# Kernel tuning notes

Measured on AMD Instinct MI355X. Metric: run time of the kernel, lower is better.

## Reference

```python
import jax, jax.numpy as jnp
import numpy as np

N_NODES = 100000
N_EDGES = 1600000
N_GRAPHS = 1024
F = 128
L = 3  # num_gnn_layers
EPS = 1e-5


def _ln(x, g, b):
    mu = jnp.mean(x, axis=-1, keepdims=True)
    v = jnp.mean((x - mu) ** 2, axis=-1, keepdims=True)
    return (x - mu) * jax.lax.rsqrt(v + EPS) * g + b


def setup_inputs() -> dict:
    key = jax.random.key(0)
    ks = jax.random.split(key, 40)
    s = 0.05
    d = {}
    d['x'] = jax.random.normal(ks[0], (N_NODES, F), jnp.float32)
    d['w'] = jax.random.uniform(ks[1], (N_NODES, 1), jnp.float32)
    d['edge_index'] = jax.random.randint(ks[2], (2, N_EDGES), 0, N_NODES)
    d['batch'] = jnp.sort(jax.random.randint(ks[3], (N_NODES,), 0, N_GRAPHS))
    # input linear: (monomer_features+1) -> gc_features
    d['W_in'] = jax.random.normal(ks[4], (F + 1, F), jnp.float32) * s
    d['b_in'] = jnp.zeros((F,), jnp.float32)
    # stacked GCBlock params [L, ...]
    d['sage_Wl'] = jax.random.normal(ks[5], (L, F, F), jnp.float32) * s
    d['sage_bl'] = jnp.zeros((L, F), jnp.float32)
    d['sage_Wr'] = jax.random.normal(ks[6], (L, F, F), jnp.float32) * s
    d['ln1_g'] = jnp.ones((L, F), jnp.float32)
    d['ln1_b'] = jnp.zeros((L, F), jnp.float32)
    d['lin1_W'] = jax.random.normal(ks[7], (L, F, F), jnp.float32) * s
    d['lin1_b'] = jnp.zeros((L, F), jnp.float32)
    d['lin2_W'] = jax.random.normal(ks[8], (L, F, F), jnp.float32) * s
    d['lin2_b'] = jnp.zeros((L, F), jnp.float32)
    d['ln2_g'] = jnp.ones((L, F), jnp.float32)
    d['ln2_b'] = jnp.zeros((L, F), jnp.float32)
    # MeanDiffFeatureBlock: Linear(2F -> F)
    d['mdf_W'] = jax.random.normal(ks[9], (2 * F, F), jnp.float32) * s
    d['mdf_b'] = jnp.zeros((F,), jnp.float32)
    # mean PoolingLayer params
    d['pln1_g'] = jnp.ones((F,), jnp.float32)
    d['pln1_b'] = jnp.zeros((F,), jnp.float32)
    d['plin1_W'] = jax.random.normal(ks[10], (F, F), jnp.float32) * s
    d['plin1_b'] = jnp.zeros((F,), jnp.float32)
    d['plin2_W'] = jax.random.normal(ks[11], (F, F), jnp.float32) * s
    d['plin2_b'] = jnp.zeros((F,), jnp.float32)
    d['pln2_g'] = jnp.ones((F,), jnp.float32)
    d['pln2_b'] = jnp.zeros((F,), jnp.float32)
    return d


def reference(x, w, edge_index, batch, W_in, b_in, sage_Wl, sage_bl, sage_Wr,
              ln1_g, ln1_b, lin1_W, lin1_b, lin2_W, lin2_b, ln2_g, ln2_b,
              mdf_W, mdf_b, pln1_g, pln1_b, plin1_W, plin1_b, plin2_W, plin2_b,
              pln2_g, pln2_b):
    src, dst = edge_index[0], edge_index[1]
    # in-degree for SAGE mean aggregation (clamped so isolated nodes -> 0 agg)
    deg = jax.ops.segment_sum(jnp.ones((N_EDGES,), jnp.float32), dst,
                              num_segments=N_NODES)
    deg = jnp.maximum(deg, 1.0)[:, None]
    # graph sizes for global_mean_pool
    cnt = jax.ops.segment_sum(jnp.ones((N_NODES,), jnp.float32), batch,
                              num_segments=N_GRAPHS)
    cnt = jnp.maximum(cnt, 1.0)[:, None]

    # inilinear on [x, weight-fraction]  (scalers are identity at init)
    h = jnp.concatenate([x, w], axis=-1) @ W_in + b_in  # [N, F]

    def gc_block(h, p):
        Wl, bl, Wr, g1, b1, W1, bb1, W2, bb2, g2, b2 = p
        # SAGEConv: lin_l(mean_j x_j) + lin_r(x_i)
        agg = jax.ops.segment_sum(h[src], dst, num_segments=N_NODES) / deg
        y = agg @ Wl + bl + h @ Wr
        y1 = _ln(y + h, g1, b1)
        y2 = jax.nn.elu(y1 @ W1 + bb1) @ W2 + bb2  # dropout = identity (eval)
        return _ln(y2 + y1, g2, b2), None

    h, _ = jax.lax.scan(gc_block, h,
                        (sage_Wl, sage_bl, sage_Wr, ln1_g, ln1_b,
                         lin1_W, lin1_b, lin2_W, lin2_b, ln2_g, ln2_b))

    # MeanDiffFeatureBlock
    gm = jax.ops.segment_sum(h, batch, num_segments=N_GRAPHS) / cnt  # [B, F]
    h = jnp.concatenate([h, h - gm[batch]], axis=-1) @ mdf_W + mdf_b

    # mean PoolingLayer
    p = jax.ops.segment_sum(h, batch, num_segments=N_GRAPHS) / cnt  # [B, F]
    hh = _ln(p, pln1_g, pln1_b)
    y = jax.nn.elu(hh @ plin1_W + plin1_b) @ plin2_W + plin2_b
    return _ln(y + hh, pln2_g, pln2_b)  # [B, F]
```

## Files before the change

### kernel.cpp

```cpp
#include <hip/hip_runtime.h>
#include <math.h>

#define NN 100000
#define NE 1600000
#define NG 1024
#define FF 128
#define BSH 9
#define NBK ((NN + 511) >> BSH)
#define RB 256
#define BCAP 16384

typedef __attribute__((ext_vector_type(8))) short short8;
typedef __attribute__((ext_vector_type(4))) float f32x4;
typedef __attribute__((ext_vector_type(2))) float f32x2;

__device__ __forceinline__ unsigned short f2b(float f) {
    union { float f; unsigned u; } v; v.f = f;
    unsigned r = (v.u + 0x7FFF + ((v.u >> 16) & 1)) >> 16;
    return (unsigned short)r;
}
__device__ __forceinline__ float us2f(unsigned short u) {
    union { unsigned u; float f; } v; v.u = ((unsigned)u) << 16; return v.f;
}
__device__ __forceinline__ float fast_elu(float v) {
    float e = __builtin_amdgcn_exp2f(v * 1.44269504088896340736f) - 1.0f;
    return v > 0.f ? v : e;
}
__device__ __forceinline__ uint2 pk8(const float* v) {
    unsigned lo = 0, hi = 0;
    lo = (unsigned)__builtin_amdgcn_cvt_pk_fp8_f32(v[0], v[1], (int)lo, false);
    lo = (unsigned)__builtin_amdgcn_cvt_pk_fp8_f32(v[2], v[3], (int)lo, true);
    hi = (unsigned)__builtin_amdgcn_cvt_pk_fp8_f32(v[4], v[5], (int)hi, false);
    hi = (unsigned)__builtin_amdgcn_cvt_pk_fp8_f32(v[6], v[7], (int)hi, true);
    uint2 r; r.x = lo; r.y = hi; return r;
}
#define MFMA(a, b, c) __builtin_amdgcn_mfma_f32_16x16x32_bf16((a), (b), (c), 0, 0, 0)

__global__ __launch_bounds__(256)
void radix_scatter(const int* __restrict__ src, const int* __restrict__ dst,
                   int* __restrict__ bcur, unsigned* __restrict__ pairs, int n) {
    __shared__ int base[NBK];
    __shared__ int cnt[NBK];
    for (int i = threadIdx.x; i < NBK; i += 256) cnt[i] = 0;
    __syncthreads();
    const int per = (n + RB - 1) / RB;
    const int beg = blockIdx.x * per;
    const int end = min(n, beg + per);
    for (int i = beg + threadIdx.x; i < end; i += 256)
        atomicAdd(&cnt[dst[i] >> BSH], 1);
    __syncthreads();
    for (int i = threadIdx.x; i < NBK; i += 256)
        base[i] = cnt[i] ? atomicAdd(&bcur[i], cnt[i]) : 0;
    __syncthreads();
    for (int i = beg + threadIdx.x; i < end; i += 256) {
        int d = dst[i];
        int p = atomicAdd(&base[d >> BSH], 1);
        pairs[p] = ((unsigned)src[i] << BSH) | (unsigned)(d & 511);
    }
}

__global__ __launch_bounds__(256)
void bucket_build(const unsigned* __restrict__ pairs, const int* __restrict__ bcur,
                  int* __restrict__ row_beg, int* __restrict__ row_end,
                  float* __restrict__ inv_deg, int* __restrict__ ssrc) {
    __shared__ int cnt[512];
    __shared__ int curs[512];
    __shared__ int wsum[4];
    const int b = blockIdx.x;
    const int n0 = b << BSH;
    const int t = threadIdx.x;
    const int lane = t & 63, wid = t >> 6;

    for (int i = t; i < 512; i += 256) cnt[i] = 0;
    __syncthreads();
    const int beg = b * BCAP, end = bcur[b];
    for (int i = beg + t; i < end; i += 256)
        atomicAdd(&cnt[pairs[i] & 511], 1);
    __syncthreads();

    int c0 = cnt[2 * t], c1 = cnt[2 * t + 1];
    int v = c0 + c1;
    int x = v;
    #pragma unroll
    for (int o = 1; o < 64; o <<= 1) {
        int y = __shfl_up(x, o);
        if (lane >= o) x += y;
    }
    if (lane == 63) wsum[wid] = x;
    __syncthreads();
    if (t == 0) {
        int s = 0;
        #pragma unroll
        for (int w2 = 0; w2 < 4; ++w2) { int tv = wsum[w2]; wsum[w2] = s; s += tv; }
    }
    __syncthreads();
    int g0 = beg + wsum[wid] + x - v;
    int g1 = g0 + c0;
    curs[2 * t] = g0;
    curs[2 * t + 1] = g1;
    {
        int node = n0 + 2 * t;
        if (node < NN) {
            row_beg[node] = g0; row_end[node] = g1;
            inv_deg[node] = 1.0f / (float)(c0 > 1 ? c0 : 1);
        }
        node = n0 + 2 * t + 1;
        if (node < NN) {
            row_beg[node] = g1; row_end[node] = g1 + c1;
            inv_deg[node] = 1.0f / (float)(c1 > 1 ? c1 : 1);
        }
    }
    __syncthreads();
    for (int i = beg + t; i < end; i += 256) {
        unsigned pr = pairs[i];
        int p = atomicAdd(&curs[pr & 511], 1);
        ssrc[p] = (int)(pr >> BSH) << 7;
    }
}

__global__ __launch_bounds__(256)
void graph_offsets(const int* __restrict__ batch, int* __restrict__ g_off,
                   float* __restrict__ inv_cnt, int* __restrict__ bcur) {
    int g = blockIdx.x * blockDim.x + threadIdx.x;
    if (g < NBK) bcur[g] = g * BCAP;
    if (g > NG) return;
    if (g == NG) { g_off[NG] = NN; return; }
    int lo = 0, hi = NN;
    while (lo < hi) { int mid = (lo + hi) >> 1; if (batch[mid] < g) lo = mid + 1; else hi = mid; }
    int lo2 = lo, hi2 = NN;
    while (lo2 < hi2) { int mid = (lo2 + hi2) >> 1; if (batch[mid] < g + 1) lo2 = mid + 1; else hi2 = mid; }
    g_off[g] = lo;
    int c = lo2 - lo;
    inv_cnt[g] = 1.0f / (float)(c > 1 ? c : 1);
}

struct WTab { const float* a[16]; };
__global__ __launch_bounds__(256)
void prep_weights(WTab tab, unsigned short* __restrict__ dst) {
    int w = blockIdx.x >> 6;
    int idx = ((blockIdx.x & 63) << 8) + threadIdx.x;
    int j = idx & 7, lane = (idx >> 3) & 63, nt = (idx >> 9) & 7, kc = idx >> 12;
    int cb = lane & 15, rq = lane >> 4;
    int k = kc * 32 + rq * 8 + j;
    int n = nt * 16 + cb;
    dst[(size_t)w * 16384 + idx] = f2b(tab.a[w][k * 128 + n]);
}

__global__ __launch_bounds__(256)
void sage_agg(const unsigned char* __restrict__ h8, const int* __restrict__ row_beg,
              const int* __restrict__ row_end, const float* __restrict__ inv_deg,
              const int* __restrict__ ssrc, unsigned short* __restrict__ aggb) {
    const int wid = threadIdx.x >> 6;
    const int lane = threadIdx.x & 63;
    const int node = blockIdx.x * 4 + wid;
    const int eg = lane >> 4, j = lane & 15;
    const int jo = j * 8;
    const int beg = row_beg[node], end = row_end[node];
    f32x2 a0 = {0.f, 0.f}, a1 = {0.f, 0.f}, a2 = {0.f, 0.f}, a3 = {0.f, 0.f};
    for (int e = beg + eg; e < end; e += 32) {
        uint2 u[8];
        #pragma unroll
        for (int k = 0; k < 8; ++k) {
            int ek = e + 4 * k;
            bool ok = ek < end;
            int idx = ssrc[ok ? ek : e];
            uint2 uu = *(const uint2*)(h8 + (unsigned)(idx + jo));
            uu.x = ok ? uu.x : 0u;
            uu.y = ok ? uu.y : 0u;
            u[k] = uu;
        }
        #pragma unroll
        for (int k = 0; k < 8; ++k) {
            a0 += __builtin_amdgcn_cvt_pk_f32_fp8(u[k].x, false);
            a1 += __builtin_amdgcn_cvt_pk_f32_fp8(u[k].x, true);
            a2 += __builtin_amdgcn_cvt_pk_f32_fp8(u[k].y, false);
            a3 += __builtin_amdgcn_cvt_pk_f32_fp8(u[k].y, true);
        }
    }
    float af[8] = {a0.x, a0.y, a1.x, a1.y, a2.x, a2.y, a3.x, a3.y};
    #pragma unroll
    for (int k = 0; k < 8; ++k) {
        af[k] += __shfl_xor(af[k], 16);
        af[k] += __shfl_xor(af[k], 32);
    }
    if (eg == 0) {
        float id = inv_deg[node];
        #pragma unroll
        for (int nt = 0; nt < 8; ++nt)
            aggb[(size_t)node * 128 + nt * 16 + j] = f2b(af[nt] * id);
    }
}

__global__ __launch_bounds__(64)
void pool_mean_b(const unsigned short* __restrict__ src, const int* __restrict__ g_off,
                 const float* __restrict__ inv_cnt, float* __restrict__ out) {
    const int g = blockIdx.x;
    const int lane = threadIdx.x & 63;
    const int j = lane & 15, rs = lane >> 4;
    const int beg = g_off[g], end = g_off[g + 1];
    float s[8] = {0.f, 0.f, 0.f, 0.f, 0.f, 0.f, 0.f, 0.f};
    for (int n = beg + rs; n < end; n += 4) {
        short8 v = *(const short8*)&src[(size_t)n * FF + j * 8];
        #pragma unroll
        for (int i = 0; i < 8; ++i) s[i] += us2f((unsigned short)v[i]);
    }
    #pragma unroll
    for (int i = 0; i < 8; ++i) {
        s[i] += __shfl_xor(s[i], 16);
        s[i] += __shfl_xor(s[i], 32);
    }
    if (rs == 0) {
        float ic = inv_cnt[g];
        #pragma unroll
        for (int i = 0; i < 8; ++i) out[(size_t)g * FF + j * 8 + i] = s[i] * ic;
    }
}

template<bool AB16, bool R1, int RESM, int ACT, bool LN, bool OF32, bool OB16, bool OB8>
__global__ __launch_bounds__(256)
void gemm_mfma(const void* __restrict__ A_,
               const unsigned short* __restrict__ Wf,
               const float* __restrict__ bias,
               const float* __restrict__ rvec, const float* __restrict__ rrow,
               const float* __restrict__ res,
               const float* __restrict__ lng, const float* __restrict__ lnb,
               float* __restrict__ outf, unsigned short* __restrict__ outb,
               unsigned char* __restrict__ outb8, int M) {
    __shared__ short Al[64 * 136];

    const int t = threadIdx.x;
    const int lane = t & 63, wid = t >> 6;
    const int m0 = blockIdx.x * 64;
    const int cb = lane & 15, rq = lane >> 4;

    if (AB16) {
        const unsigned short* Ab = (const unsigned short*)A_;
        for (int i = t; i < 1024; i += 256) {
            int row = i >> 4, seg = i & 15;
            int gr = m0 + row; if (gr >= M) gr = M - 1;
            *(uint4*)&Al[row * 136 + seg * 8] = *(const uint4*)&Ab[(size_t)gr * 128 + seg * 8];
        }
    } else {
        const float* Af = (const float*)A_;
        for (int i = t; i < 2048; i += 256) {
            int row = i >> 5, seg = i & 31;
            int gr = m0 + row; if (gr >= M) gr = M - 1;
            float4 v = *(const float4*)&Af[(size_t)gr * 128 + seg * 4];
            ushort4 o = {f2b(v.x), f2b(v.y), f2b(v.z), f2b(v.w)};
            *(ushort4*)&Al[row * 136 + seg * 4] = o;
        }
    }
    __syncthreads();

    f32x4 acc[8];
    #pragma unroll
    for (int nt = 0; nt < 8; ++nt) acc[nt] = (f32x4){0.f, 0.f, 0.f, 0.f};

    const int aoff_base = (wid * 16 + cb) * 136 + rq * 8;
    for (int kc = 0; kc < 4; ++kc) {
        short8 a0 = *(const short8*)&Al[aoff_base + kc * 32];
        #pragma unroll
        for (int nt = 0; nt < 8; ++nt) {
            short8 b0 = *(const short8*)&Wf[(size_t)(kc * 8 + nt) * 512 + lane * 8];
            acc[nt] = MFMA(a0, b0, acc[nt]);
        }
    }

    float bs[8], rr[8], lg[8], lb[8];
    #pragma unroll
    for (int nt = 0; nt < 8; ++nt) {
        int col = nt * 16 + cb;
        bs[nt] = bias[col];
        if (R1) rr[nt] = rrow[col];
        if (LN) { lg[nt] = lng[col]; lb[nt] = lnb[col]; }
    }
    #pragma unroll
    for (int reg = 0; reg < 4; ++reg) {
        int m = m0 + wid * 16 + rq * 4 + reg;
        int mc = m < M ? m : M - 1;
        float v[8];
        #pragma unroll
        for (int nt = 0; nt < 8; ++nt) v[nt] = acc[nt][reg] + bs[nt];
        if (R1) {
            float rv = rvec[mc];
            #pragma unroll
            for (int nt = 0; nt < 8; ++nt) v[nt] += rv * rr[nt];
        }
        if (RESM == 1) {
            #pragma unroll
            for (int nt = 0; nt < 8; ++nt) v[nt] += res[(size_t)mc * 128 + nt * 16 + cb];
        }
        if (ACT == 1) {
            #pragma unroll
            for (int nt = 0; nt < 8; ++nt) v[nt] = fast_elu(v[nt]);
        }
        if (LN) {
            float s1 = 0.f, s2 = 0.f;
            #pragma unroll
            for (int nt = 0; nt < 8; ++nt) { s1 += v[nt]; s2 += v[nt] * v[nt]; }
            #pragma unroll
            for (int o = 8; o >= 1; o >>= 1) { s1 += __shfl_xor(s1, o); s2 += __shfl_xor(s2, o); }
            float mu = s1 * (1.f / 128.f);
            float rs = rsqrtf(s2 * (1.f / 128.f) - mu * mu + 1e-5f);
            #pragma unroll
            for (int nt = 0; nt < 8; ++nt) v[nt] = (v[nt] - mu) * rs * lg[nt] + lb[nt];
        }
        if (m < M) {
            #pragma unroll
            for (int nt = 0; nt < 8; ++nt) {
                size_t o = (size_t)m * 128 + nt * 16 + cb;
                if (OF32) outf[o] = v[nt];
                if (OB16) outb[o] = f2b(v[nt]);
            }
            if (OB8) *(uint2*)&outb8[(size_t)m * 128 + cb * 8] = pk8(v);
        }
    }
}

__global__ __launch_bounds__(256)
void gc_chain(const unsigned short* __restrict__ hin, const unsigned short* __restrict__ aggb,
              unsigned short* __restrict__ hout, unsigned char* __restrict__ h8out,
              const unsigned short* __restrict__ Wl_f, const unsigned short* __restrict__ Wr_f,
              const unsigned short* __restrict__ W1_f, const unsigned short* __restrict__ W2_f,
              const float* __restrict__ bl,
              const float* __restrict__ g1, const float* __restrict__ b1,
              const float* __restrict__ bb1, const float* __restrict__ bb2,
              const float* __restrict__ g2, const float* __restrict__ b2, int M) {
    __shared__ short Hl[64 * 136];
    __shared__ short Gl[64 * 136];

    const int t = threadIdx.x;
    const int lane = t & 63, wid = t >> 6;
    const int m0 = blockIdx.x * 64;
    const int cb = lane & 15, rq = lane >> 4;
    const int aoff_base = (wid * 16 + cb) * 136 + rq * 8;
    const int boff = lane * 8;

    for (int i = t; i < 1024; i += 256) {
        int row = i >> 4, seg = i & 15;
        int gr = m0 + row; if (gr >= M) gr = M - 1;
        *(uint4*)&Hl[row * 136 + seg * 8] = *(const uint4*)&hin[(size_t)gr * 128 + seg * 8];
        *(uint4*)&Gl[row * 136 + seg * 8] = *(const uint4*)&aggb[(size_t)gr * 128 + seg * 8];
    }
    __syncthreads();

    f32x4 acc[8];
    #pragma unroll
    for (int nt = 0; nt < 8; ++nt) acc[nt] = (f32x4){0.f, 0.f, 0.f, 0.f};

    for (int kc = 0; kc < 4; ++kc) {
        short8 a0 = *(const short8*)&Gl[aoff_base + kc * 32];
        short8 a1 = *(const short8*)&Hl[aoff_base + kc * 32];
        #pragma unroll
        for (int nt = 0; nt < 8; ++nt) {
            const size_t wo = (size_t)(kc * 8 + nt) * 512 + boff;
            acc[nt] = MFMA(a0, *(const short8*)&Wl_f[wo], acc[nt]);
            acc[nt] = MFMA(a1, *(const short8*)&Wr_f[wo], acc[nt]);
        }
    }

    float y1r[4][8];
    {
        float bs[8], lg[8], lb[8];
        #pragma unroll
        for (int nt = 0; nt < 8; ++nt) {
            int col = nt * 16 + cb;
            bs[nt] = bl[col]; lg[nt] = g1[col]; lb[nt] = b1[col];
        }
        #pragma unroll
        for (int reg = 0; reg < 4; ++reg) {
            int r = wid * 16 + rq * 4 + reg;
            float v[8];
            float s1 = 0.f, s2 = 0.f;
            #pragma unroll
            for (int nt = 0; nt < 8; ++nt) {
                v[nt] = acc[nt][reg] + bs[nt] + us2f((unsigned short)Hl[r * 136 + nt * 16 + cb]);
                s1 += v[nt]; s2 += v[nt] * v[nt];
            }
            #pragma unroll
            for (int o = 8; o >= 1; o >>= 1) { s1 += __shfl_xor(s1, o); s2 += __shfl_xor(s2, o); }
            float mu = s1 * (1.f / 128.f);
            float rs = rsqrtf(s2 * (1.f / 128.f) - mu * mu + 1e-5f);
            #pragma unroll
            for (int nt = 0; nt < 8; ++nt) {
                float y = (v[nt] - mu) * rs * lg[nt] + lb[nt];
                y1r[reg][nt] = y;
                Hl[r * 136 + nt * 16 + cb] = (short)f2b(y);
            }
        }
    }

    #pragma unroll
    for (int nt = 0; nt < 8; ++nt) acc[nt] = (f32x4){0.f, 0.f, 0.f, 0.f};
    for (int kc = 0; kc < 4; ++kc) {
        short8 a0 = *(const short8*)&Hl[aoff_base + kc * 32];
        #pragma unroll
        for (int nt = 0; nt < 8; ++nt)
            acc[nt] = MFMA(a0, *(const short8*)&W1_f[(size_t)(kc * 8 + nt) * 512 + boff], acc[nt]);
    }
    {
        float bs[8];
        #pragma unroll
        for (int nt = 0; nt < 8; ++nt) bs[nt] = bb1[nt * 16 + cb];
        #pragma unroll
        for (int reg = 0; reg < 4; ++reg) {
            int r = wid * 16 + rq * 4 + reg;
            #pragma unroll
            for (int nt = 0; nt < 8; ++nt) {
                float v = fast_elu(acc[nt][reg] + bs[nt]);
                Gl[r * 136 + nt * 16 + cb] = (short)f2b(v);
            }
        }
    }

    #pragma unroll
    for (int nt = 0; nt < 8; ++nt) acc[nt] = (f32x4){0.f, 0.f, 0.f, 0.f};
    for (int kc = 0; kc < 4; ++kc) {
        short8 a0 = *(const short8*)&Gl[aoff_base + kc * 32];
        #pragma unroll
        for (int nt = 0; nt < 8; ++nt)
            acc[nt] = MFMA(a0, *(const short8*)&W2_f[(size_t)(kc * 8 + nt) * 512 + boff], acc[nt]);
    }
    {
        float bs[8], lg[8], lb[8];
        #pragma unroll
        for (int nt = 0; nt < 8; ++nt) {
            int col = nt * 16 + cb;
            bs[nt] = bb2[col]; lg[nt] = g2[col]; lb[nt] = b2[col];
        }
        #pragma unroll
        for (int reg = 0; reg < 4; ++reg) {
            int r = wid * 16 + rq * 4 + reg;
            int m = m0 + r;
            float v[8];
            float s1 = 0.f, s2 = 0.f;
            #pragma unroll
            for (int nt = 0; nt < 8; ++nt) {
                v[nt] = acc[nt][reg] + bs[nt] + y1r[reg][nt];
                s1 += v[nt]; s2 += v[nt] * v[nt];
            }
            #pragma unroll
            for (int o = 8; o >= 1; o >>= 1) { s1 += __shfl_xor(s1, o); s2 += __shfl_xor(s2, o); }
            float mu = s1 * (1.f / 128.f);
            float rs = rsqrtf(s2 * (1.f / 128.f) - mu * mu + 1e-5f);
            if (m < M) {
                float fv[8];
                #pragma unroll
                for (int nt = 0; nt < 8; ++nt) {
                    fv[nt] = (v[nt] - mu) * rs * lg[nt] + lb[nt];
                    hout[(size_t)m * 128 + nt * 16 + cb] = f2b(fv[nt]);
                }
                *(uint2*)&h8out[(size_t)m * 128 + cb * 8] = pk8(fv);
            }
        }
    }
}

__global__ __launch_bounds__(256)
void head_chain(const float* __restrict__ gm,
                const unsigned short* __restrict__ Wa_f,
                const unsigned short* __restrict__ P1_f,
                const unsigned short* __restrict__ P2_f,
                const float* __restrict__ mdfb,
                const float* __restrict__ g1, const float* __restrict__ b1,
                const float* __restrict__ p1b, const float* __restrict__ p2b,
                const float* __restrict__ g2, const float* __restrict__ b2,
                float* __restrict__ outp) {
    __shared__ short Al[64 * 136];

    const int t = threadIdx.x;
    const int lane = t & 63, wid = t >> 6;
    const int m0 = blockIdx.x * 64;
    const int cb = lane & 15, rq = lane >> 4;
    const int aoff_base = (wid * 16 + cb) * 136 + rq * 8;
    const int boff = lane * 8;

    for (int i = t; i < 2048; i += 256) {
        int row = i >> 5, seg = i & 31;
        float4 v = *(const float4*)&gm[(size_t)(m0 + row) * 128 + seg * 4];
        ushort4 o = {f2b(v.x), f2b(v.y), f2b(v.z), f2b(v.w)};
        *(ushort4*)&Al[row * 136 + seg * 4] = o;
    }
    __syncthreads();

    f32x4 acc[8];
    #pragma unroll
    for (int nt = 0; nt < 8; ++nt) acc[nt] = (f32x4){0.f, 0.f, 0.f, 0.f};
    for (int kc = 0; kc < 4; ++kc) {
        short8 a0 = *(const short8*)&Al[aoff_base + kc * 32];
        #pragma unroll
        for (int nt = 0; nt < 8; ++nt)
            acc[nt] = MFMA(a0, *(const short8*)&Wa_f[(size_t)(kc * 8 + nt) * 512 + boff], acc[nt]);
    }
    float y1r[4][8];
    {
        float bs[8], lg[8], lb[8];
        #pragma unroll
        for (int nt = 0; nt < 8; ++nt) {
            int col = nt * 16 + cb;
            bs[nt] = mdfb[col]; lg[nt] = g1[col]; lb[nt] = b1[col];
        }
        #pragma unroll
        for (int reg = 0; reg < 4; ++reg) {
            int r = wid * 16 + rq * 4 + reg;
            float v[8];
            float s1 = 0.f, s2 = 0.f;
            #pragma unroll
            for (int nt = 0; nt < 8; ++nt) {
                v[nt] = acc[nt][reg] + bs[nt];
                s1 += v[nt]; s2 += v[nt] * v[nt];
            }
            #pragma unroll
            for (int o = 8; o >= 1; o >>= 1) { s1 += __shfl_xor(s1, o); s2 += __shfl_xor(s2, o); }
            float mu = s1 * (1.f / 128.f);
            float rs = rsqrtf(s2 * (1.f / 128.f) - mu * mu + 1e-5f);
            #pragma unroll
            for (int nt = 0; nt < 8; ++nt) {
                float y = (v[nt] - mu) * rs * lg[nt] + lb[nt];
                y1r[reg][nt] = y;
                Al[r * 136 + nt * 16 + cb] = (short)f2b(y);
            }
        }
    }

    #pragma unroll
    for (int nt = 0; nt < 8; ++nt) acc[nt] = (f32x4){0.f, 0.f, 0.f, 0.f};
    for (int kc = 0; kc < 4; ++kc) {
        short8 a0 = *(const short8*)&Al[aoff_base + kc * 32];
        #pragma unroll
        for (int nt = 0; nt < 8; ++nt)
            acc[nt] = MFMA(a0, *(const short8*)&P1_f[(size_t)(kc * 8 + nt) * 512 + boff], acc[nt]);
    }
    {
        float bs[8];
        #pragma unroll
        for (int nt = 0; nt < 8; ++nt) bs[nt] = p1b[nt * 16 + cb];
        #pragma unroll
        for (int reg = 0; reg < 4; ++reg) {
            int r = wid * 16 + rq * 4 + reg;
            #pragma unroll
            for (int nt = 0; nt < 8; ++nt) {
                float v = fast_elu(acc[nt][reg] + bs[nt]);
                Al[r * 136 + nt * 16 + cb] = (short)f2b(v);
            }
        }
    }

    #pragma unroll
    for (int nt = 0; nt < 8; ++nt) acc[nt] = (f32x4){0.f, 0.f, 0.f, 0.f};
    for (int kc = 0; kc < 4; ++kc) {
        short8 a0 = *(const short8*)&Al[aoff_base + kc * 32];
        #pragma unroll
        for (int nt = 0; nt < 8; ++nt)
            acc[nt] = MFMA(a0, *(const short8*)&P2_f[(size_t)(kc * 8 + nt) * 512 + boff], acc[nt]);
    }
    {
        float bs[8], lg[8], lb[8];
        #pragma unroll
        for (int nt = 0; nt < 8; ++nt) {
            int col = nt * 16 + cb;
            bs[nt] = p2b[col]; lg[nt] = g2[col]; lb[nt] = b2[col];
        }
        #pragma unroll
        for (int reg = 0; reg < 4; ++reg) {
            int r = wid * 16 + rq * 4 + reg;
            int m = m0 + r;
            float v[8];
            float s1 = 0.f, s2 = 0.f;
            #pragma unroll
            for (int nt = 0; nt < 8; ++nt) {
                v[nt] = acc[nt][reg] + bs[nt] + y1r[reg][nt];
                s1 += v[nt]; s2 += v[nt] * v[nt];
            }
            #pragma unroll
            for (int o = 8; o >= 1; o >>= 1) { s1 += __shfl_xor(s1, o); s2 += __shfl_xor(s2, o); }
            float mu = s1 * (1.f / 128.f);
            float rs = rsqrtf(s2 * (1.f / 128.f) - mu * mu + 1e-5f);
            #pragma unroll
            for (int nt = 0; nt < 8; ++nt)
                outp[(size_t)m * 128 + nt * 16 + cb] = (v[nt] - mu) * rs * lg[nt] + lb[nt];
        }
    }
}

extern "C" void kernel_launch(void* const* d_in, const int* in_sizes, int n_in,
                              void* d_out, int out_size, void* d_ws, size_t ws_size,
                              hipStream_t stream) {
    const float* x      = (const float*)d_in[0];
    const float* w      = (const float*)d_in[1];
    const int*   ei     = (const int*)d_in[2];
    const int*   batch  = (const int*)d_in[3];
    const float* W_in   = (const float*)d_in[4];
    const float* b_in   = (const float*)d_in[5];
    const float* sage_Wl = (const float*)d_in[6];
    const float* sage_bl = (const float*)d_in[7];
    const float* sage_Wr = (const float*)d_in[8];
    const float* ln1_g  = (const float*)d_in[9];
    const float* ln1_b  = (const float*)d_in[10];
    const float* lin1_W = (const float*)d_in[11];
    const float* lin1_b = (const float*)d_in[12];
    const float* lin2_W = (const float*)d_in[13];
    const float* lin2_b = (const float*)d_in[14];
    const float* ln2_g  = (const float*)d_in[15];
    const float* ln2_b  = (const float*)d_in[16];
    const float* mdf_W  = (const float*)d_in[17];
    const float* mdf_b  = (const float*)d_in[18];
    const float* pln1_g = (const float*)d_in[19];
    const float* pln1_b = (const float*)d_in[20];
    const float* plin1_W = (const float*)d_in[21];
    const float* plin1_b = (const float*)d_in[22];
    const float* plin2_W = (const float*)d_in[23];
    const float* plin2_b = (const float*)d_in[24];
    const float* pln2_g = (const float*)d_in[25];
    const float* pln2_b = (const float*)d_in[26];
    float* out = (float*)d_out;

    const int* e_src = ei;
    const int* e_dst = ei + NE;

    float* ws = (float*)d_ws;
    size_t off = 0;
    float* gm    = ws + off; off += (size_t)NG * FF;
    float* hh    = ws + off; off += (size_t)NG * FF;
    float* tt    = ws + off; off += (size_t)NG * FF;
    float* inv_deg = ws + off; off += NN;
    float* inv_cnt = ws + off; off += NG;
    unsigned short* us = (unsigned short*)(ws + off);
    size_t uoff = 0;
    unsigned short* hb0  = us + uoff; uoff += (size_t)NN * FF;
    unsigned short* hb1  = us + uoff; uoff += (size_t)NN * FF;
    unsigned short* aggb = us + uoff; uoff += (size_t)NN * FF;
    unsigned short* wt   = us + uoff; uoff += (size_t)16 * 16384;
    int* iw = (int*)(us + uoff);
    size_t ioff = 0;
    unsigned* pairs = (unsigned*)iw; ioff += (size_t)NBK * BCAP;
    int* ssrc    = iw + ioff; ioff += (size_t)NBK * BCAP;
    int* row_beg = iw + ioff; ioff += NN;
    int* row_end = iw + ioff; ioff += NN;
    int* g_off   = iw + ioff; ioff += NG + 1;
    int* bcur    = iw + ioff; ioff += NBK;
    unsigned char* h8 = (unsigned char*)pairs;

    WTab tab;
    tab.a[0] = W_in;
    for (int l = 0; l < 3; ++l) {
        tab.a[1 + l]  = sage_Wl + (size_t)l * 16384;
        tab.a[4 + l]  = sage_Wr + (size_t)l * 16384;
        tab.a[7 + l]  = lin1_W + (size_t)l * 16384;
        tab.a[10 + l] = lin2_W + (size_t)l * 16384;
    }
    tab.a[13] = mdf_W;
    tab.a[14] = plin1_W;
    tab.a[15] = plin2_W;
    prep_weights<<<16 * 64, 256, 0, stream>>>(tab, wt);
    const unsigned short* win_t = wt + 0 * 16384;
    const unsigned short* wa_t  = wt + 13 * 16384;
    const unsigned short* p1_t  = wt + 14 * 16384;
    const unsigned short* p2_t  = wt + 15 * 16384;

    graph_offsets<<<(NG + 256) / 256, 256, 0, stream>>>(batch, g_off, inv_cnt, bcur);
    radix_scatter<<<RB, 256, 0, stream>>>(e_src, e_dst, bcur, pairs, NE);
    bucket_build<<<NBK, 256, 0, stream>>>(pairs, bcur, row_beg, row_end, inv_deg, ssrc);

    const int GN = (NN + 63) / 64;
    const int GB = NG / 64;

    gemm_mfma<false, true, 0, 0, false, false, true, true><<<GN, 256, 0, stream>>>(
        x, win_t, b_in, w, W_in + 128 * 128,
        nullptr, nullptr, nullptr, nullptr, hb0, h8, NN);

    unsigned short* hcur = hb0;
    unsigned short* hnxt = hb1;
    for (int l = 0; l < 3; ++l) {
        sage_agg<<<NN / 4, 256, 0, stream>>>(h8, row_beg, row_end, inv_deg, ssrc, aggb);
        gc_chain<<<GN, 256, 0, stream>>>(
            hcur, aggb, hnxt, h8,
            wt + (size_t)(1 + l) * 16384, wt + (size_t)(4 + l) * 16384,
            wt + (size_t)(7 + l) * 16384, wt + (size_t)(10 + l) * 16384,
            sage_bl + (size_t)l * FF,
            ln1_g + (size_t)l * FF, ln1_b + (size_t)l * FF,
            lin1_b + (size_t)l * FF, lin2_b + (size_t)l * FF,
            ln2_g + (size_t)l * FF, ln2_b + (size_t)l * FF, NN);
        unsigned short* tmp = hcur; hcur = hnxt; hnxt = tmp;
    }

    pool_mean_b<<<NG, 64, 0, stream>>>(hcur, g_off, inv_cnt, gm);
    head_chain<<<GB, 256, 0, stream>>>(
        gm, wa_t, p1_t, p2_t, mdf_b,
        pln1_g, pln1_b, plin1_b, plin2_b, pln2_g, pln2_b, out);
    (void)hh; (void)tt;
}
```

Baseline: 513.8 us.

## Process two nodes per wave in aggregation and widen bucket/pool kernels

The SAGE aggregation now has each wavefront gather two destination nodes at once, interleaving their loads so more memory requests are in flight. Out-of-range lanes read a dummy index 0, and ssrc[0] is zeroed up front so that read stays defined. bucket_build moves to 512 threads, one node per thread, and radix_scatter uses twice as many blocks. pool_mean_b uses four waves per graph with a shared-memory reduction. Pairing nodes can waste work when the two degrees differ.

New measurement: 504.5 us. Within noise of the previous version (-1.8%).

```diff
diff --git a/kernel.cpp b/kernel.cpp
--- a/kernel.cpp
+++ b/kernel.cpp
@@ -7,7 +7,7 @@
 #define FF 128
 #define BSH 9
 #define NBK ((NN + 511) >> BSH)
-#define RB 256
+#define RB 512
 #define BCAP 16384
 
 typedef __attribute__((ext_vector_type(8))) short short8;
@@ -59,28 +59,27 @@
     }
 }
 
-__global__ __launch_bounds__(256)
+__global__ __launch_bounds__(512)
 void bucket_build(const unsigned* __restrict__ pairs, const int* __restrict__ bcur,
                   int* __restrict__ row_beg, int* __restrict__ row_end,
                   float* __restrict__ inv_deg, int* __restrict__ ssrc) {
     __shared__ int cnt[512];
     __shared__ int curs[512];
-    __shared__ int wsum[4];
+    __shared__ int wsum[8];
     const int b = blockIdx.x;
     const int n0 = b << BSH;
     const int t = threadIdx.x;
     const int lane = t & 63, wid = t >> 6;
 
-    for (int i = t; i < 512; i += 256) cnt[i] = 0;
+    cnt[t] = 0;
     __syncthreads();
     const int beg = b * BCAP, end = bcur[b];
-    for (int i = beg + t; i < end; i += 256)
+    for (int i = beg + t; i < end; i += 512)
         atomicAdd(&cnt[pairs[i] & 511], 1);
     __syncthreads();
 
-    int c0 = cnt[2 * t], c1 = cnt[2 * t + 1];
-    int v = c0 + c1;
-    int x = v;
+    int c = cnt[t];
+    int x = c;
     #pragma unroll
     for (int o = 1; o < 64; o <<= 1) {
         int y = __shfl_up(x, o);
@@ -91,27 +90,20 @@
     if (t == 0) {
         int s = 0;
         #pragma unroll
-        for (int w2 = 0; w2 < 4; ++w2) { int tv = wsum[w2]; wsum[w2] = s; s += tv; }
-    }
-    __syncthreads();
-    int g0 = beg + wsum[wid] + x - v;
-    int g1 = g0 + c0;
-    curs[2 * t] = g0;
-    curs[2 * t + 1] = g1;
+        for (int w2 = 0; w2 < 8; ++w2) { int tv = wsum[w2]; wsum[w2] = s; s += tv; }
+    }
+    __syncthreads();
+    int g0 = beg + wsum[wid] + x - c;
+    curs[t] = g0;
     {
-        int node = n0 + 2 * t;
+        int node = n0 + t;
         if (node < NN) {
-            row_beg[node] = g0; row_end[node] = g1;
-            inv_deg[node] = 1.0f / (float)(c0 > 1 ? c0 : 1);
-        }
-        node = n0 + 2 * t + 1;
-        if (node < NN) {
-            row_beg[node] = g1; row_end[node] = g1 + c1;
-            inv_deg[node] = 1.0f / (float)(c1 > 1 ? c1 : 1);
-        }
-    }
-    __syncthreads();
-    for (int i = beg + t; i < end; i += 256) {
+            row_beg[node] = g0; row_end[node] = g0 + c;
+            inv_deg[node] = 1.0f / (float)(c > 1 ? c : 1);
+        }
+    }
+    __syncthreads();
+    for (int i = beg + t; i < end; i += 512) {
         unsigned pr = pairs[i];
         int p = atomicAdd(&curs[pr & 511], 1);
         ssrc[p] = (int)(pr >> BSH) << 7;
@@ -120,8 +112,10 @@
 
 __global__ __launch_bounds__(256)
 void graph_offsets(const int* __restrict__ batch, int* __restrict__ g_off,
-                   float* __restrict__ inv_cnt, int* __restrict__ bcur) {
+                   float* __restrict__ inv_cnt, int* __restrict__ bcur,
+                   int* __restrict__ ssrc) {
     int g = blockIdx.x * blockDim.x + threadIdx.x;
+    if (g == 0) ssrc[0] = 0;
     if (g < NBK) bcur[g] = g * BCAP;
     if (g > NG) return;
     if (g == NG) { g_off[NG] = NN; return; }
@@ -152,54 +146,82 @@
               const int* __restrict__ ssrc, unsigned short* __restrict__ aggb) {
     const int wid = threadIdx.x >> 6;
     const int lane = threadIdx.x & 63;
-    const int node = blockIdx.x * 4 + wid;
+    const int n0 = blockIdx.x * 8 + wid * 2;
+    const int n1 = n0 + 1;
     const int eg = lane >> 4, j = lane & 15;
     const int jo = j * 8;
-    const int beg = row_beg[node], end = row_end[node];
+    const int beg0 = row_beg[n0], end0 = row_end[n0];
+    const int beg1 = row_beg[n1], end1 = row_end[n1];
     f32x2 a0 = {0.f, 0.f}, a1 = {0.f, 0.f}, a2 = {0.f, 0.f}, a3 = {0.f, 0.f};
-    for (int e = beg + eg; e < end; e += 32) {
-        uint2 u[8];
+    f32x2 b0 = {0.f, 0.f}, b1 = {0.f, 0.f}, b2 = {0.f, 0.f}, b3 = {0.f, 0.f};
+    int e0 = beg0 + eg, e1 = beg1 + eg;
+    const int d0 = end0 - beg0, d1 = end1 - beg1;
+    const int nit = ((d0 > d1 ? d0 : d1) + 31) >> 5;
+    for (int it = 0; it < nit; ++it, e0 += 32, e1 += 32) {
+        uint2 u0[8], u1[8];
         #pragma unroll
         for (int k = 0; k < 8; ++k) {
-            int ek = e + 4 * k;
-            bool ok = ek < end;
-            int idx = ssrc[ok ? ek : e];
+            int ek = e0 + 4 * k;
+            bool ok = ek < end0;
+            int idx = ssrc[ok ? ek : 0];
             uint2 uu = *(const uint2*)(h8 + (unsigned)(idx + jo));
             uu.x = ok ? uu.x : 0u;
             uu.y = ok ? uu.y : 0u;
-            u[k] = uu;
+            u0[k] = uu;
         }
         #pragma unroll
         for (int k = 0; k < 8; ++k) {
-            a0 += __builtin_amdgcn_cvt_pk_f32_fp8(u[k].x, false);
-            a1 += __builtin_amdgcn_cvt_pk_f32_fp8(u[k].x, true);
-            a2 += __builtin_amdgcn_cvt_pk_f32_fp8(u[k].y, false);
-            a3 += __builtin_amdgcn_cvt_pk_f32_fp8(u[k].y, true);
+            int ek = e1 + 4 * k;
+            bool ok = ek < end1;
+            int idx = ssrc[ok ? ek : 0];
+            uint2 uu = *(const uint2*)(h8 + (unsigned)(idx + jo));
+            uu.x = ok ? uu.x : 0u;
+            uu.y = ok ? uu.y : 0u;
+            u1[k] = uu;
+        }
+        #pragma unroll
+        for (int k = 0; k < 8; ++k) {
+            a0 += __builtin_amdgcn_cvt_pk_f32_fp8(u0[k].x, false);
+            a1 += __builtin_amdgcn_cvt_pk_f32_fp8(u0[k].x, true);
+            a2 += __builtin_amdgcn_cvt_pk_f32_fp8(u0[k].y, false);
+            a3 += __builtin_amdgcn_cvt_pk_f32_fp8(u0[k].y, true);
+            b0 += __builtin_amdgcn_cvt_pk_f32_fp8(u1[k].x, false);
+            b1 += __builtin_amdgcn_cvt_pk_f32_fp8(u1[k].x, true);
+            b2 += __builtin_amdgcn_cvt_pk_f32_fp8(u1[k].y, false);
+            b3 += __builtin_amdgcn_cvt_pk_f32_fp8(u1[k].y, true);
         }
     }
     float af[8] = {a0.x, a0.y, a1.x, a1.y, a2.x, a2.y, a3.x, a3.y};
+    float bf[8] = {b0.x, b0.y, b1.x, b1.y, b2.x, b2.y, b3.x, b3.y};
     #pragma unroll
     for (int k = 0; k < 8; ++k) {
         af[k] += __shfl_xor(af[k], 16);
         af[k] += __shfl_xor(af[k], 32);
+        bf[k] += __shfl_xor(bf[k], 16);
+        bf[k] += __shfl_xor(bf[k], 32);
     }
     if (eg == 0) {
-        float id = inv_deg[node];
-        #pragma unroll
-        for (int nt = 0; nt < 8; ++nt)
-            aggb[(size_t)node * 128 + nt * 16 + j] = f2b(af[nt] * id);
-    }
-}
-
-__global__ __launch_bounds__(64)
+        float id0 = inv_deg[n0];
+        float id1 = inv_deg[n1];
+        #pragma unroll
+        for (int nt = 0; nt < 8; ++nt) {
+            aggb[(size_t)n0 * 128 + nt * 16 + j] = f2b(af[nt] * id0);
+            aggb[(size_t)n1 * 128 + nt * 16 + j] = f2b(bf[nt] * id1);
+        }
+    }
+}
+
+__global__ __launch_bounds__(256)
 void pool_mean_b(const unsigned short* __restrict__ src, const int* __restrict__ g_off,
                  const float* __restrict__ inv_cnt, float* __restrict__ out) {
+    __shared__ float red[3][128];
     const int g = blockIdx.x;
-    const int lane = threadIdx.x & 63;
+    const int t = threadIdx.x;
+    const int lane = t & 63, wid = t >> 6;
     const int j = lane & 15, rs = lane >> 4;
     const int beg = g_off[g], end = g_off[g + 1];
     float s[8] = {0.f, 0.f, 0.f, 0.f, 0.f, 0.f, 0.f, 0.f};
-    for (int n = beg + rs; n < end; n += 4) {
+    for (int n = beg + rs + wid * 4; n < end; n += 16) {
         short8 v = *(const short8*)&src[(size_t)n * FF + j * 8];
         #pragma unroll
         for (int i = 0; i < 8; ++i) s[i] += us2f((unsigned short)v[i]);
@@ -209,10 +231,18 @@
         s[i] += __shfl_xor(s[i], 16);
         s[i] += __shfl_xor(s[i], 32);
     }
-    if (rs == 0) {
+    if (wid > 0 && rs == 0) {
+        #pragma unroll
+        for (int i = 0; i < 8; ++i) red[wid - 1][j * 8 + i] = s[i];
+    }
+    __syncthreads();
+    if (wid == 0 && rs == 0) {
         float ic = inv_cnt[g];
         #pragma unroll
-        for (int i = 0; i < 8; ++i) out[(size_t)g * FF + j * 8 + i] = s[i] * ic;
+        for (int i = 0; i < 8; ++i) {
+            float v = s[i] + red[0][j * 8 + i] + red[1][j * 8 + i] + red[2][j * 8 + i];
+            out[(size_t)g * FF + j * 8 + i] = v * ic;
+        }
     }
 }
 
@@ -658,9 +688,9 @@
     const unsigned short* p1_t  = wt + 14 * 16384;
     const unsigned short* p2_t  = wt + 15 * 16384;
 
-    graph_offsets<<<(NG + 256) / 256, 256, 0, stream>>>(batch, g_off, inv_cnt, bcur);
+    graph_offsets<<<(NG + 256) / 256, 256, 0, stream>>>(batch, g_off, inv_cnt, bcur, ssrc);
     radix_scatter<<<RB, 256, 0, stream>>>(e_src, e_dst, bcur, pairs, NE);
-    bucket_build<<<NBK, 256, 0, stream>>>(pairs, bcur, row_beg, row_end, inv_deg, ssrc);
+    bucket_build<<<NBK, 512, 0, stream>>>(pairs, bcur, row_beg, row_end, inv_deg, ssrc);
 
     const int GN = (NN + 63) / 64;
     const int GB = NG / 64;
@@ -672,7 +702,7 @@
     unsigned short* hcur = hb0;
     unsigned short* hnxt = hb1;
     for (int l = 0; l < 3; ++l) {
-        sage_agg<<<NN / 4, 256, 0, stream>>>(h8, row_beg, row_end, inv_deg, ssrc, aggb);
+        sage_agg<<<NN / 8, 256, 0, stream>>>(h8, row_beg, row_end, inv_deg, ssrc, aggb);
         gc_chain<<<GN, 256, 0, stream>>>(
             hcur, aggb, hnxt, h8,
             wt + (size_t)(1 + l) * 16384, wt + (size_t)(4 + l) * 16384,
@@ -684,7 +714,7 @@
         unsigned short* tmp = hcur; hcur = hnxt; hnxt = tmp;
     }
 
-    pool_mean_b<<<NG, 64, 0, stream>>>(hcur, g_off, inv_cnt, gm);
+    pool_mean_b<<<NG, 256, 0, stream>>>(hcur, g_off, inv_cnt, gm);
     head_chain<<<GB, 256, 0, stream>>>(
         gm, wa_t, p1_t, p2_t, mdf_b,
         pln1_g, pln1_b, plin1_b, plin2_b, pln2_g, pln2_b, out);
```
